# Kernel optimization log

Measured on AMD Instinct MI355X. Metric: run time of the kernel, lower is better.

The kernel has to match this reference:

```python
import jax, jax.numpy as jnp
import numpy as np

BETA = 0.25  # commitment cost (init kwarg)


def setup_inputs() -> dict:
    key = jax.random.key(0)
    k1, k2 = jax.random.split(key)
    B, C, H, W = 8, 256, 64, 64
    K = 8192  # codebook_size
    z = jax.random.normal(k1, (B, C, H, W), dtype=jnp.float32)
    # torch init is uniform(-1/K, 1/K); use same scale
    codebook = jax.random.uniform(k2, (K, C), dtype=jnp.float32,
                                  minval=-1.0 / K, maxval=1.0 / K)
    return {"z": z, "codebook": codebook}


def reference(z, codebook):
    # z: [B, C, H, W] -> [B, H, W, C]
    z_bhwc = jnp.transpose(z, (0, 2, 3, 1))
    D = codebook.shape[1]
    zf = z_bhwc.reshape(-1, D)  # [N, D]
    # squared euclidean distances: ||z||^2 + ||e||^2 - 2 z.e  -> [N, K]
    d = (jnp.sum(zf * zf, axis=1, keepdims=True)
         + jnp.sum(codebook * codebook, axis=1)
         - 2.0 * jnp.einsum('nd,kd->nk', zf, codebook))
    min_encoding_indices = jnp.argmin(d, axis=1)  # [N]
    z_q = codebook[min_encoding_indices].reshape(z_bhwc.shape)  # [B,H,W,C]
    sg = jax.lax.stop_gradient
    # legacy=False branch
    loss = (BETA * jnp.mean((sg(z_q) - z_bhwc) ** 2)
            + jnp.mean((z_q - sg(z_bhwc)) ** 2))
    # straight-through estimator
    z_q = z_bhwc + sg(z_q - z_bhwc)
    z_q = jnp.transpose(z_q, (0, 3, 1, 2))  # back to [B, C, H, W]
    return z_q, loss, min_encoding_indices
```

## Files before the change

kernel.cpp:

```cpp
#include <hip/hip_runtime.h>
#include <hip/hip_bf16.h>
#include <math.h>

typedef unsigned short u16;
typedef unsigned int u32;
typedef unsigned long long u64;
typedef __attribute__((ext_vector_type(8))) _Float16 f16x8;
typedef __attribute__((ext_vector_type(4))) float f32x4;

#define B_   8
#define C_   256
#define HW_  4096
#define N_   32768
#define K_   8192

#define O_LOSSP 0ULL
#define O_E2    16384ULL
#define O_ZN2   49152ULL
#define O_IDX   180224ULL
#define O_ZT    311296ULL
#define O_AP    33865728ULL
#define O_BP    50642944ULL
#define O_CAND  54837248ULL
#define WS_NEED 88391680ULL

#define THRESH_T 9e-5f

#define GSWZ(r) (((r) >> 1) & 3)

__device__ __forceinline__ u16 f2h(float f) {
    _Float16 h = (_Float16)f;
    return __builtin_bit_cast(u16, h);
}

__device__ __forceinline__ void gload16(const void* g, void* l) {
    __builtin_amdgcn_global_load_lds((const __attribute__((address_space(1))) void*)g,
                                     (__attribute__((address_space(3))) void*)l, 16, 0, 0);
}


__global__ __launch_bounds__(256) void vq_prep(const float* __restrict__ z,
                                               const float* __restrict__ cb,
                                               float* __restrict__ zT,
                                               u16* __restrict__ Ap,
                                               u16* __restrict__ Bp,
                                               float* __restrict__ zn2g,
                                               float* __restrict__ e2g) {
    __shared__ float zl[128][65];
    const int tid = threadIdx.x;

    if (blockIdx.x < 128) {
        const int k0 = blockIdx.x * 64;
        const int r = tid >> 2;
        const int u4 = tid & 3;
        const int k = k0 + r;
        const int r7 = k & 127;
        double eacc = 0.0;
        #pragma unroll
        for (int kc8 = 0; kc8 < 8; ++kc8) {
            const float* src = cb + (size_t)k * C_ + kc8 * 32 + u4 * 8;
            float4 v0 = *(const float4*)(src);
            float4 v1 = *(const float4*)(src + 4);
            float vals[8] = { v0.x, v0.y, v0.z, v0.w, v1.x, v1.y, v1.z, v1.w };
            u16 tmp[8];
            #pragma unroll
            for (int j = 0; j < 8; ++j) {
                eacc += (double)vals[j] * (double)vals[j];
                tmp[j] = f2h(vals[j] * 8192.0f);
            }
            char* dst = (char*)Bp + ((size_t)((k >> 7) * 8 + kc8)) * 8192
                      + r7 * 64 + ((u4 * 16) ^ (GSWZ(r7) << 4));
            *(uint4*)dst = *(uint4*)tmp;
        }
        eacc += __shfl_xor(eacc, 1);
        eacc += __shfl_xor(eacc, 2);
        if (u4 == 0) e2g[k] = (float)eacc;
        return;
    }

    const int bidz = blockIdx.x - 128;
    const int bb = bidz >> 6;
    const int hwc = bidz & 63;
    const int hw0 = hwc * 64;
    const int n0 = bb * HW_ + hw0;
    const int lane = tid & 63, wid = tid >> 6;
    const int r = tid >> 2;
    const int u4 = tid & 3;
    const int n = n0 + r;
    const int r7 = n & 127;
    double zacc = 0.0;

    for (int h = 0; h < 2; ++h) {
        __syncthreads();
        for (int c0 = 0; c0 < 128; c0 += 4) {
            int c = c0 + (tid >> 6);
            zl[c][tid & 63] = z[((size_t)(bb * C_ + h * 128 + c)) * HW_ + hw0 + (tid & 63)];
        }
        __syncthreads();
        for (int it = 0; it < 8; ++it) {
            int rp = it * 8 + wid * 2 + (lane >> 5);
            int c4 = (lane & 31) * 4;
            float4 v = { zl[c4][rp], zl[c4 + 1][rp], zl[c4 + 2][rp], zl[c4 + 3][rp] };
            *(float4*)(zT + (size_t)(n0 + rp) * C_ + h * 128 + c4) = v;
        }
        #pragma unroll
        for (int q = 0; q < 4; ++q) {
            u16 tmp[8];
            #pragma unroll
            for (int j = 0; j < 8; ++j) {
                float f = zl[q * 32 + u4 * 8 + j][r];
                zacc += (double)f * (double)f;
                tmp[j] = f2h(f);
            }
            char* dst = (char*)Ap + ((size_t)((n >> 7) * 8 + h * 4 + q)) * 8192
                      + r7 * 64 + ((u4 * 16) ^ (GSWZ(r7) << 4));
            *(uint4*)dst = *(uint4*)tmp;
        }
    }
    zacc += __shfl_xor(zacc, 1);
    zacc += __shfl_xor(zacc, 2);
    if (u4 == 0) zn2g[n] = (float)zacc;
}

__global__ __launch_bounds__(512) void vq_gemm_top2(const u16* __restrict__ Ap,
                                                    const u16* __restrict__ Bp,
                                                    u32* __restrict__ cand) {
    __shared__ char lds[49152];
    const int tid = threadIdx.x;
    const int lane = tid & 63, wid = tid >> 6;
    const int wm = wid >> 2, wn = wid & 3;
    const int l15 = lane & 15, l4 = lane >> 4;

    const int raw = blockIdx.x;
    const int m_tile = raw >> 6;
    const int n_tile = (raw & 7) * 8 + ((raw >> 3) & 7);

    f32x4 acc[4][4];
    #pragma unroll
    for (int i = 0; i < 4; ++i)
        #pragma unroll
        for (int j = 0; j < 4; ++j) acc[i][j] = (f32x4){0.f, 0.f, 0.f, 0.f};

    int rc[4], rz[4], xc[4], xz[4];
    #pragma unroll
    for (int f = 0; f < 4; ++f) {
        rc[f] = wm * 64 + f * 16 + l15;
        rz[f] = wn * 64 + f * 16 + l15;
        xc[f] = GSWZ(rc[f]) << 4;
        xz[f] = GSWZ(rz[f]) << 4;
    }
    const int ob = l4 * 16;

    const char* codes_src = (const char*)Bp + (size_t)n_tile * 65536;
    const char* z_src     = (const char*)Ap + (size_t)m_tile * 131072;

    #define STAGE(buf, kc)                                                        \
        do {                                                                      \
            const char* cs_ = codes_src + (size_t)(kc) * 8192;                    \
            const char* ze_ = z_src + (size_t)(kc) * 8192;              \
            const char* zo_ = z_src + 65536 + (size_t)(kc) * 8192;      \
            char* lb_ = lds + (buf) * 24576;                                      \
            gload16(cs_ + tid * 16, lb_ + tid * 16);                              \
            gload16(ze_ + tid * 16, lb_ + 8192 + tid * 16);                       \
            gload16(zo_ + tid * 16, lb_ + 16384 + tid * 16);                      \
        } while (0)

    #define COMPUTE(buf)                                                          \
        do {                                                                      \
            const char* base_ = lds + (buf) * 24576;                              \
            f16x8 la[4], lb[4];                                                   \
            _Pragma("unroll")                                                     \
            for (int f = 0; f < 4; ++f) {                                         \
                la[f] = *(const f16x8*)(base_ + rc[f] * 64 + (ob ^ xc[f]));       \
                lb[f] = *(const f16x8*)(base_ + 8192 + rz[f] * 64 + (ob ^ xz[f]));\
            }                                                                     \
            _Pragma("unroll")                                                     \
            for (int fm = 0; fm < 4; ++fm)                                        \
                _Pragma("unroll")                                                 \
                for (int fn = 0; fn < 4; ++fn)                                    \
                    acc[fm][fn] = __builtin_amdgcn_mfma_f32_16x16x32_f16(         \
                        la[fm], lb[fn], acc[fm][fn], 0, 0, 0);                    \
        } while (0)

    STAGE(0, 0);
    #pragma unroll
    for (int kc = 0; kc < 8; ++kc) {
        __syncthreads();
        if (kc < 7) STAGE((kc + 1) & 1, kc + 1);
        COMPUTE(kc & 1);
    }

    #undef STAGE
    #undef COMPUTE

    const int ktile = n_tile * 2 + wm;
    #pragma unroll
    for (int fn = 0; fn < 4; ++fn) {
        u32 m1 = 0xFFFFFFFFu, m2 = 0xFFFFFFFFu;
        #pragma unroll
        for (int fm = 0; fm < 4; ++fm) {
            #pragma unroll
            for (int rv = 0; rv < 4; ++rv) {
                float w = fmaf(acc[fm][fn][rv], -0x1p-12f, 0.5f);
                u32 p = (__float_as_uint(w) & ~63u) | (u32)(fm * 16 + l4 * 4 + rv);
                u32 t = m1 > p ? m1 : p;
                m1 = m1 < p ? m1 : p;
                m2 = m2 < t ? m2 : t;
            }
        }
        #pragma unroll
        for (int off = 16; off <= 32; off <<= 1) {
            u32 b1 = __shfl_xor(m1, off);
            u32 b2 = __shfl_xor(m2, off);
            u32 t = m1 > b1 ? m1 : b1;
            m1 = m1 < b1 ? m1 : b1;
            u32 s2 = m2 < b2 ? m2 : b2;
            m2 = s2 < t ? s2 : t;
        }
        if (l4 == 0) {
            int rowg = m_tile * 256 + wn * 64 + fn * 16 + l15;
            *(uint2*)(cand + (size_t)rowg * 256 + ktile * 2) = make_uint2(m1, m2);
        }
    }
}

__global__ __launch_bounds__(256) void vq_pick(const u32* __restrict__ cand,
                                               const float* __restrict__ zT,
                                               const float* __restrict__ cb,
                                               const float* __restrict__ e2g,
                                               const float* __restrict__ zn2g,
                                               int* __restrict__ idxg,
                                               float* __restrict__ out) {
    const int lane = threadIdx.x & 63, wid = threadIdx.x >> 6;
    const int row = blockIdx.x * 4 + wid;
    const uint4 e = ((const uint4*)(cand + (size_t)row * 256))[lane];
    u32 m = e.x < e.y ? e.x : e.y;
    u32 mzw = e.z < e.w ? e.z : e.w;
    m = m < mzw ? m : mzw;
    #pragma unroll
    for (int off = 32; off >= 1; off >>= 1) {
        u32 o = __shfl_xor(m, off);
        m = o < m ? o : m;
    }
    const float thr = __uint_as_float(m & ~63u) + THRESH_T;
    const u32 ev[4] = { e.x, e.y, e.z, e.w };
    u64 msk[4];
    int tot = 0;
    #pragma unroll
    for (int j = 0; j < 4; ++j) {
        msk[j] = __ballot(__uint_as_float(ev[j] & ~63u) <= thr);
        tot += __popcll((unsigned long long)msk[j]);
    }
    int bk;
    if (tot == 1) {
        const int j = msk[0] ? 0 : (msk[1] ? 1 : (msk[2] ? 2 : 3));
        const int l = __ffsll((unsigned long long)msk[j]) - 1;
        const u32 val = __shfl(ev[j], l);
        bk = ((l * 4 + j) >> 1) * 64 + (int)(val & 63u);
    } else {
        const float4 zv = *(const float4*)(zT + (size_t)row * C_ + lane * 4);
        const float zn2a = zn2g[row];
        float bd = INFINITY;
        bk = 0x7fffffff;
        #pragma unroll
        for (int j = 0; j < 4; ++j) {
            u64 mj = msk[j];
            while (mj) {
                const int l = __ffsll((unsigned long long)mj) - 1;
                mj &= mj - 1;
                const u32 val = __shfl(ev[j], l);
                const int k = ((l * 4 + j) >> 1) * 64 + (int)(val & 63u);
                const float4 cv = *(const float4*)(cb + (size_t)k * C_ + lane * 4);
                double s = (double)zv.x * cv.x + (double)zv.y * cv.y
                         + (double)zv.z * cv.z + (double)zv.w * cv.w;
                #pragma unroll
                for (int off = 32; off >= 1; off >>= 1) s += __shfl_xor(s, off);
                const float sf = (float)s;
                const float d = (zn2a + e2g[k]) - 2.0f * sf;
                if (d < bd || (d == bd && k < bk)) { bd = d; bk = k; }
            }
        }
    }
    if (lane == 0) {
        idxg[row] = bk;
        out[8388609 + row] = (float)bk;
    }
}

__global__ __launch_bounds__(256) void vq_zq_loss_kernel(const float* __restrict__ z,
                                                         const float* __restrict__ cb,
                                                         const int* __restrict__ idxg,
                                                         float* __restrict__ out,
                                                         double* __restrict__ partial) {
    double acc = 0.0;
    for (size_t i4 = (size_t)blockIdx.x * 256 + threadIdx.x; i4 < 2097152ULL;
         i4 += 2048ULL * 256ULL) {
        const size_t i = i4 * 4;
        const int hw = (int)(i & 4095);
        const int bc = (int)(i >> 12);
        const int c = bc & 255;
        const int b = bc >> 8;
        const int n = (b << 12) + hw;
        const float4 zv = *(const float4*)(z + i);
        const int k0 = idxg[n], k1 = idxg[n + 1], k2 = idxg[n + 2], k3 = idxg[n + 3];
        const float t0 = cb[(size_t)k0 * C_ + c] - zv.x;
        const float t1 = cb[(size_t)k1 * C_ + c] - zv.y;
        const float t2 = cb[(size_t)k2 * C_ + c] - zv.z;
        const float t3 = cb[(size_t)k3 * C_ + c] - zv.w;
        float4 o = { zv.x + t0, zv.y + t1, zv.z + t2, zv.w + t3 };
        *(float4*)(out + i) = o;
        acc += (double)t0 * t0 + (double)t1 * t1 + (double)t2 * t2 + (double)t3 * t3;
    }
    #pragma unroll
    for (int off = 32; off >= 1; off >>= 1) acc += __shfl_xor(acc, off);
    __shared__ double ls[4];
    const int lane = threadIdx.x & 63, wid = threadIdx.x >> 6;
    if (lane == 0) ls[wid] = acc;
    __syncthreads();
    if (threadIdx.x == 0) partial[blockIdx.x] = ls[0] + ls[1] + ls[2] + ls[3];
}

__global__ __launch_bounds__(256) void vq_loss_final(const double* __restrict__ partial,
                                                     float* __restrict__ out) {
    double acc = 0.0;
    for (int j = threadIdx.x; j < 2048; j += 256) acc += partial[j];
    #pragma unroll
    for (int off = 32; off >= 1; off >>= 1) acc += __shfl_xor(acc, off);
    __shared__ double ls[4];
    const int lane = threadIdx.x & 63, wid = threadIdx.x >> 6;
    if (lane == 0) ls[wid] = acc;
    __syncthreads();
    if (threadIdx.x == 0)
        out[8388608] = (float)(1.25 * (ls[0] + ls[1] + ls[2] + ls[3]) / 8388608.0);
}

__global__ __launch_bounds__(256) void vq_e2_old(const float* __restrict__ cb,
                                                 float* __restrict__ e2g) {
    int lane = threadIdx.x & 63;
    int w = threadIdx.x >> 6;
    int k = blockIdx.x * 4 + w;
    const float4 v = *reinterpret_cast<const float4*>(cb + (size_t)k * C_ + lane * 4);
    double acc = (double)v.x * v.x + (double)v.y * v.y
               + (double)v.z * v.z + (double)v.w * v.w;
    #pragma unroll
    for (int off = 32; off >= 1; off >>= 1) acc += __shfl_xor(acc, off);
    if (lane == 0) e2g[k] = (float)acc;
}

__global__ __launch_bounds__(256) void vq_zn2_old(const float* __restrict__ z,
                                                  float* __restrict__ zn2g) {
    int n = blockIdx.x * 256 + threadIdx.x;
    int b = n >> 12;
    int hw = n & 4095;
    const float* p = z + (size_t)b * C_ * HW_ + hw;
    double acc = 0.0;
    #pragma unroll 8
    for (int c = 0; c < C_; ++c) {
        float v = p[(size_t)c * HW_];
        acc += (double)v * (double)v;
    }
    zn2g[n] = (float)acc;
}

__global__ __launch_bounds__(256) void vq_argmin_old(const float* __restrict__ z,
                                                     const float* __restrict__ cb,
                                                     const float* __restrict__ e2g,
                                                     const float* __restrict__ zn2g,
                                                     int* __restrict__ idxg) {
    __shared__ float zt[C_][32];
    __shared__ float et[64][64];
    const int tid = threadIdx.x;
    const int n0 = blockIdx.x * 32;
    const int b = n0 >> 12;
    const int hw0 = n0 & 4095;
    {
        const int nn = tid & 31;
        const int c8 = tid >> 5;
        #pragma unroll
        for (int j = 0; j < 32; ++j) {
            const int c = j * 8 + c8;
            zt[c][nn] = z[(size_t)(b * C_ + c) * HW_ + hw0 + nn];
        }
    }
    const int cg = tid & 15;
    const int rg = tid >> 4;
    const int r0 = rg * 2;
    __syncthreads();
    const float zn2a = zn2g[n0 + r0];
    const float zn2b = zn2g[n0 + r0 + 1];
    float dmin0 = INFINITY, dmin1 = INFINITY;
    int imin0 = 0, imin1 = 0;
    const int kk = tid >> 2;
    const int c4 = (tid & 3) * 16;
    for (int kt = 0; kt < K_; kt += 64) {
        double s00 = 0, s01 = 0, s02 = 0, s03 = 0;
        double s10 = 0, s11 = 0, s12 = 0, s13 = 0;
        for (int cc = 0; cc < C_; cc += 64) {
            __syncthreads();
            {
                const float* src = cb + (size_t)(kt + kk) * C_ + cc + c4;
                #pragma unroll
                for (int j = 0; j < 16; j += 4) {
                    const float4 v = *reinterpret_cast<const float4*>(src + j);
                    et[c4 + j + 0][kk] = v.x;
                    et[c4 + j + 1][kk] = v.y;
                    et[c4 + j + 2][kk] = v.z;
                    et[c4 + j + 3][kk] = v.w;
                }
            }
            __syncthreads();
            #pragma unroll 4
            for (int c2 = 0; c2 < 64; ++c2) {
                const float2 zv = *reinterpret_cast<const float2*>(&zt[cc + c2][r0]);
                const float4 ev = *reinterpret_cast<const float4*>(&et[c2][cg * 4]);
                const double z0 = (double)zv.x, z1 = (double)zv.y;
                s00 += z0 * ev.x; s01 += z0 * ev.y; s02 += z0 * ev.z; s03 += z0 * ev.w;
                s10 += z1 * ev.x; s11 += z1 * ev.y; s12 += z1 * ev.z; s13 += z1 * ev.w;
            }
        }
        const int kbase = kt + cg * 4;
        const float sf0[4] = {(float)s00, (float)s01, (float)s02, (float)s03};
        const float sf1[4] = {(float)s10, (float)s11, (float)s12, (float)s13};
        #pragma unroll
        for (int j = 0; j < 4; ++j) {
            const int k = kbase + j;
            const float e2k = e2g[k];
            const float d0 = (zn2a + e2k) - 2.0f * sf0[j];
            const float d1 = (zn2b + e2k) - 2.0f * sf1[j];
            if (d0 < dmin0) { dmin0 = d0; imin0 = k; }
            if (d1 < dmin1) { dmin1 = d1; imin1 = k; }
        }
    }
    #pragma unroll
    for (int off = 8; off >= 1; off >>= 1) {
        const float od0 = __shfl_xor(dmin0, off);
        const int   oi0 = __shfl_xor(imin0, off);
        const float od1 = __shfl_xor(dmin1, off);
        const int   oi1 = __shfl_xor(imin1, off);
        if (od0 < dmin0 || (od0 == dmin0 && oi0 < imin0)) { dmin0 = od0; imin0 = oi0; }
        if (od1 < dmin1 || (od1 == dmin1 && oi1 < imin1)) { dmin1 = od1; imin1 = oi1; }
    }
    if (cg == 0) {
        idxg[n0 + r0]     = imin0;
        idxg[n0 + r0 + 1] = imin1;
    }
}

__global__ __launch_bounds__(256) void vq_final_old(const int* __restrict__ idxg,
                                                    float* __restrict__ out) {
    const int i = blockIdx.x * 256 + threadIdx.x;
    out[8388609 + i] = (float)idxg[i];
}

extern "C" void kernel_launch(void* const* d_in, const int* in_sizes, int n_in,
                              void* d_out, int out_size, void* d_ws, size_t ws_size,
                              hipStream_t stream) {
    const float* z  = (const float*)d_in[0];
    const float* cb = (const float*)d_in[1];
    float* out = (float*)d_out;
    char* ws = (char*)d_ws;

    double* lossp = (double*)(ws + O_LOSSP);
    float*  e2g  = (float*)(ws + O_E2);
    float*  zn2g = (float*)(ws + O_ZN2);
    int*    idxg = (int*)(ws + O_IDX);

    if (ws_size >= WS_NEED) {
        float* zT   = (float*)(ws + O_ZT);
        u16*   Ap   = (u16*)(ws + O_AP);
        u16*   Bp   = (u16*)(ws + O_BP);
        u32*   cand = (u32*)(ws + O_CAND);

        hipLaunchKernelGGL(vq_prep, dim3(640), dim3(256), 0, stream,
                           z, cb, zT, Ap, Bp, zn2g, e2g);
        hipLaunchKernelGGL(vq_gemm_top2, dim3(8192), dim3(512), 0, stream, Ap, Bp, cand);
        hipLaunchKernelGGL(vq_pick, dim3(N_ / 4), dim3(256), 0, stream,
                           cand, zT, cb, e2g, zn2g, idxg, out);
    } else {
        hipLaunchKernelGGL(vq_e2_old, dim3(K_ / 4), dim3(256), 0, stream, cb, e2g);
        hipLaunchKernelGGL(vq_zn2_old, dim3(N_ / 256), dim3(256), 0, stream, z, zn2g);
        hipLaunchKernelGGL(vq_argmin_old, dim3(N_ / 32), dim3(256), 0, stream,
                           z, cb, e2g, zn2g, idxg);
        hipLaunchKernelGGL(vq_final_old, dim3(N_ / 256), dim3(256), 0, stream, idxg, out);
    }

    hipLaunchKernelGGL(vq_zq_loss_kernel, dim3(2048), dim3(256), 0, stream,
                       z, cb, idxg, out, lossp);
    hipLaunchKernelGGL(vq_loss_final, dim3(1), dim3(256), 0, stream, lossp, out);
}
```

Baseline: 244.8 us.

## Halve GEMM block tile and load z fragments directly into registers

The top-2 GEMM kernel now runs with 256 threads (4 waves) and a 128x128 block tile instead of 512 threads and 256x128, doubling the grid. Only the codebook tile is staged through LDS (16 KB double buffer); the z operand fragments are read straight from global memory into registers with a two-slot register double buffer. The aim is lower LDS use and higher occupancy, and dropping the z LDS round-trip. In exchange each z fragment is fetched by two waves from global/L2 with less coalesced 16-byte reads, and the codebook is reloaded twice as often overall.

```diff
diff --git a/kernel.cpp b/kernel.cpp
--- a/kernel.cpp
+++ b/kernel.cpp
@@ -122,13 +122,13 @@
     if (u4 == 0) zn2g[n] = (float)zacc;
 }
 
-__global__ __launch_bounds__(512) void vq_gemm_top2(const u16* __restrict__ Ap,
+__global__ __launch_bounds__(256) void vq_gemm_top2(const u16* __restrict__ Ap,
                                                     const u16* __restrict__ Bp,
                                                     u32* __restrict__ cand) {
-    __shared__ char lds[49152];
+    __shared__ char lds[16384];
     const int tid = threadIdx.x;
     const int lane = tid & 63, wid = tid >> 6;
-    const int wm = wid >> 2, wn = wid & 3;
+    const int wm = wid >> 1, wn = wid & 1;
     const int l15 = lane & 15, l4 = lane >> 4;
 
     const int raw = blockIdx.x;
@@ -141,56 +141,66 @@
         #pragma unroll
         for (int j = 0; j < 4; ++j) acc[i][j] = (f32x4){0.f, 0.f, 0.f, 0.f};
 
-    int rc[4], rz[4], xc[4], xz[4];
+    const int ob = l4 * 16;
+    int rc[4], xc[4], zoff[4];
     #pragma unroll
     for (int f = 0; f < 4; ++f) {
         rc[f] = wm * 64 + f * 16 + l15;
-        rz[f] = wn * 64 + f * 16 + l15;
         xc[f] = GSWZ(rc[f]) << 4;
-        xz[f] = GSWZ(rz[f]) << 4;
-    }
-    const int ob = l4 * 16;
+        const int rz = wn * 64 + f * 16 + l15;
+        zoff[f] = rz * 64 + (ob ^ (GSWZ(rz) << 4));
+    }
 
     const char* codes_src = (const char*)Bp + (size_t)n_tile * 65536;
-    const char* z_src     = (const char*)Ap + (size_t)m_tile * 131072;
+    const char* z_src     = (const char*)Ap + (size_t)m_tile * 65536;
+
+    f16x8 zf0[4], zf1[4];
 
     #define STAGE(buf, kc)                                                        \
         do {                                                                      \
             const char* cs_ = codes_src + (size_t)(kc) * 8192;                    \
-            const char* ze_ = z_src + (size_t)(kc) * 8192;              \
-            const char* zo_ = z_src + 65536 + (size_t)(kc) * 8192;      \
-            char* lb_ = lds + (buf) * 24576;                                      \
+            char* lb_ = lds + (buf) * 8192;                                       \
             gload16(cs_ + tid * 16, lb_ + tid * 16);                              \
-            gload16(ze_ + tid * 16, lb_ + 8192 + tid * 16);                       \
-            gload16(zo_ + tid * 16, lb_ + 16384 + tid * 16);                      \
+            gload16(cs_ + 4096 + tid * 16, lb_ + 4096 + tid * 16);                \
         } while (0)
 
-    #define COMPUTE(buf)                                                          \
+    #define ZLOAD(zf_, kc)                                                        \
         do {                                                                      \
-            const char* base_ = lds + (buf) * 24576;                              \
-            f16x8 la[4], lb[4];                                                   \
+            const char* zs_ = z_src + (size_t)(kc) * 8192;                        \
             _Pragma("unroll")                                                     \
-            for (int f = 0; f < 4; ++f) {                                         \
+            for (int f = 0; f < 4; ++f)                                           \
+                zf_[f] = *(const f16x8*)(zs_ + zoff[f]);                          \
+        } while (0)
+
+    #define COMPUTE(buf, zf_)                                                     \
+        do {                                                                      \
+            const char* base_ = lds + (buf) * 8192;                               \
+            f16x8 la[4];                                                          \
+            _Pragma("unroll")                                                     \
+            for (int f = 0; f < 4; ++f)                                           \
                 la[f] = *(const f16x8*)(base_ + rc[f] * 64 + (ob ^ xc[f]));       \
-                lb[f] = *(const f16x8*)(base_ + 8192 + rz[f] * 64 + (ob ^ xz[f]));\
-            }                                                                     \
             _Pragma("unroll")                                                     \
             for (int fm = 0; fm < 4; ++fm)                                        \
                 _Pragma("unroll")                                                 \
                 for (int fn = 0; fn < 4; ++fn)                                    \
                     acc[fm][fn] = __builtin_amdgcn_mfma_f32_16x16x32_f16(         \
-                        la[fm], lb[fn], acc[fm][fn], 0, 0, 0);                    \
+                        la[fm], zf_[fn], acc[fm][fn], 0, 0, 0);                   \
         } while (0)
 
     STAGE(0, 0);
-    #pragma unroll
-    for (int kc = 0; kc < 8; ++kc) {
+    ZLOAD(zf0, 0);
+    #pragma unroll
+    for (int kc = 0; kc < 8; kc += 2) {
         __syncthreads();
-        if (kc < 7) STAGE((kc + 1) & 1, kc + 1);
-        COMPUTE(kc & 1);
+        if (kc < 7) { STAGE(1, kc + 1); ZLOAD(zf1, kc + 1); }
+        COMPUTE(0, zf0);
+        __syncthreads();
+        if (kc < 6) { STAGE(0, kc + 2); ZLOAD(zf0, kc + 2); }
+        COMPUTE(1, zf1);
     }
 
     #undef STAGE
+    #undef ZLOAD
     #undef COMPUTE
 
     const int ktile = n_tile * 2 + wm;
@@ -218,7 +228,7 @@
             m2 = s2 < t ? s2 : t;
         }
         if (l4 == 0) {
-            int rowg = m_tile * 256 + wn * 64 + fn * 16 + l15;
+            int rowg = m_tile * 128 + wn * 64 + fn * 16 + l15;
             *(uint2*)(cand + (size_t)rowg * 256 + ktile * 2) = make_uint2(m1, m2);
         }
     }
@@ -473,7 +483,7 @@
 
         hipLaunchKernelGGL(vq_prep, dim3(640), dim3(256), 0, stream,
                            z, cb, zT, Ap, Bp, zn2g, e2g);
-        hipLaunchKernelGGL(vq_gemm_top2, dim3(8192), dim3(512), 0, stream, Ap, Bp, cand);
+        hipLaunchKernelGGL(vq_gemm_top2, dim3(16384), dim3(256), 0, stream, Ap, Bp, cand);
         hipLaunchKernelGGL(vq_pick, dim3(N_ / 4), dim3(256), 0, stream,
                            cand, zT, cb, e2g, zn2g, idxg, out);
     } else {
```

Result: faster. 227.3 us (-7.1%).
